# Performance work log

Measured on AMD Instinct MI355X. Metric: run time of the kernel, lower is better.

## Reference

```python
import jax, jax.numpy as jnp
import numpy as np

B, T, I, H, L = 256, 512, 64, 256, 2


def _lstm_layer(x, Wih, Whh, bih, bhh):
    # x: [B, T, Din]; Wih: [4H, Din]; Whh: [4H, H]; gate order i,f,g,o (PyTorch)
    Hdim = Whh.shape[1]
    # Precompute input projections for all timesteps (one big GEMM)
    x_proj = jnp.einsum('btd,gd->btg', x, Wih) + bih + bhh  # [B, T, 4H]
    x_proj = jnp.transpose(x_proj, (1, 0, 2))  # [T, B, 4H]

    def step(carry, xt):
        h, c = carry
        gates = xt + h @ Whh.T  # [B, 4H]
        i, f, g, o = jnp.split(gates, 4, axis=-1)
        i = jax.nn.sigmoid(i)
        f = jax.nn.sigmoid(f)
        g = jnp.tanh(g)
        o = jax.nn.sigmoid(o)
        c = f * c + i * g
        h = o * jnp.tanh(c)
        return (h, c), h

    b = x.shape[0]
    h0 = jnp.zeros((b, Hdim), dtype=x.dtype)
    c0 = jnp.zeros((b, Hdim), dtype=x.dtype)
    _, hs = jax.lax.scan(step, (h0, c0), x_proj)  # hs: [T, B, H]
    return jnp.transpose(hs, (1, 0, 2))  # [B, T, H]


def setup_inputs() -> dict:
    key = jax.random.key(0)
    ks = jax.random.split(key, 12)
    s_in = 1.0 / np.sqrt(H)
    inp = {
        'x': jax.random.normal(ks[0], (B, T, I), dtype=jnp.float32),
        'Wih0': jax.random.uniform(ks[1], (4 * H, I), minval=-s_in, maxval=s_in),
        'Whh0': jax.random.uniform(ks[2], (4 * H, H), minval=-s_in, maxval=s_in),
        'bih0': jax.random.uniform(ks[3], (4 * H,), minval=-s_in, maxval=s_in),
        'bhh0': jax.random.uniform(ks[4], (4 * H,), minval=-s_in, maxval=s_in),
        'Wih1': jax.random.uniform(ks[5], (4 * H, H), minval=-s_in, maxval=s_in),
        'Whh1': jax.random.uniform(ks[6], (4 * H, H), minval=-s_in, maxval=s_in),
        'bih1': jax.random.uniform(ks[7], (4 * H,), minval=-s_in, maxval=s_in),
        'bhh1': jax.random.uniform(ks[8], (4 * H,), minval=-s_in, maxval=s_in),
        'Wfc': jax.random.uniform(ks[9], (1, H), minval=-s_in, maxval=s_in),
        'bfc': jax.random.uniform(ks[10], (1,), minval=-s_in, maxval=s_in),
    }
    return inp


def reference(x, Wih0, Whh0, bih0, bhh0, Wih1, Whh1, bih1, bhh1, Wfc, bfc):
    h1 = _lstm_layer(x, Wih0, Whh0, bih0, bhh0)   # [B, T, H]
    h2 = _lstm_layer(h1, Wih1, Whh1, bih1, bhh1)  # [B, T, H]
    last = h2[:, -1, :]                           # [B, H]
    return last @ Wfc.T + bfc                     # [B, 1]
```

## Files before the change

### kernel.cpp

```cpp
#include <hip/hip_runtime.h>

#define TT   512
#define IDIM 64
#define HDIM 256

typedef short  short8  __attribute__((ext_vector_type(8)));
typedef short  short4v __attribute__((ext_vector_type(4)));
typedef float  f32x4   __attribute__((ext_vector_type(4)));
typedef unsigned int       u32;
typedef unsigned long long u64;

__device__ __forceinline__ short f2bf(float f) {
    unsigned u = __float_as_uint(f);
    u = u + 0x7FFFu + ((u >> 16) & 1u);
    return (short)(u >> 16);
}
__device__ __forceinline__ u32 f2bf_u(float f) {
    unsigned u = __float_as_uint(f);
    u = u + 0x7FFFu + ((u >> 16) & 1u);
    return (u >> 16);
}
__device__ __forceinline__ float bf2f(short h) {
    return __uint_as_float(((unsigned)(unsigned short)h) << 16);
}
__device__ __forceinline__ float sigm(float x)  { return 1.0f / (1.0f + __expf(-x)); }
__device__ __forceinline__ float tanh_(float x) { return 2.0f / (1.0f + __expf(-2.0f * x)) - 1.0f; }

__global__ __launch_bounds__(256, 1) void lstm_fused(
    const float* __restrict__ x,
    const float* __restrict__ Wih0, const float* __restrict__ Whh0,
    const float* __restrict__ bih0, const float* __restrict__ bhh0,
    const float* __restrict__ Wih1, const float* __restrict__ Whh1,
    const float* __restrict__ bih1, const float* __restrict__ bhh1,
    const float* __restrict__ Wfc,  const float* __restrict__ bfc,
    float* __restrict__ out, char* __restrict__ ws)
{
    u32* h0w = (u32*)ws;
    u32* h1w = h0w + 2 * 16 * 16 * 256;

    const int blk   = blockIdx.x;
    const int grp   = ((blk & 7) << 1) | ((blk >> 3) & 1);
    const int chunk = blk >> 4;
    const int tid   = threadIdx.x;
    const int lane  = tid & 63;
    const int wave  = tid >> 6;
    const int quad  = lane >> 4;
    const int nn    = lane & 15;

    __shared__ short A0[16][328];
    __shared__ short A1[16][520];
    __shared__ float gbuf[2][4][16][16];
    __shared__ float red[16][16];
    __shared__ float ldspad[13312];

    for (int i = tid; i < 16 * 328; i += 256) (&A0[0][0])[i] = 0;
    for (int i = tid; i < 16 * 520; i += 256) (&A1[0][0])[i] = 0;

    const int wrow = wave * HDIM + chunk * 16 + nn;
    short8 w0f[10];
    short8 w1f[16];
#pragma unroll
    for (int kb = 0; kb < 10; ++kb)
#pragma unroll
        for (int j = 0; j < 8; ++j) {
            int k = kb * 32 + quad * 8 + j;
            float v = (k < 64) ? Wih0[wrow * IDIM + k] : Whh0[wrow * HDIM + (k - 64)];
            w0f[kb][j] = f2bf(v);
        }
#pragma unroll
    for (int kb = 0; kb < 16; ++kb)
#pragma unroll
        for (int j = 0; j < 8; ++j) {
            int k = kb * 32 + quad * 8 + j;
            float v = (k < 256) ? Wih1[wrow * HDIM + k] : Whh1[wrow * HDIM + (k - 256)];
            w1f[kb][j] = f2bf(v);
        }
    const float bias0 = bih0[wrow] + bhh0[wrow];
    const float bias1 = bih1[wrow] + bhh1[wrow];

    const int em = tid >> 4;
    const int ej = tid & 15;
    float c0 = 0.0f, c1 = 0.0f;

    auto load_x = [&](int t) {
        const float4 v = *(const float4*)&x[((size_t)(grp * 16 + em) * TT + t) * IDIM + ej * 4];
        short4v sv;
        sv[0] = f2bf(v.x); sv[1] = f2bf(v.y); sv[2] = f2bf(v.z); sv[3] = f2bf(v.w);
        *(short4v*)&A0[em][ej * 4] = sv;
    };

    __syncthreads();
    load_x(0);
    __syncthreads();

    for (int s = 0; s <= TT; ++s) {
        const int par = s & 1;
        const u32 tag = (u32)(s + 1);

        if (s < TT) {
            f32x4 acc = {0.f, 0.f, 0.f, 0.f};
#pragma unroll
            for (int kb = 0; kb < 10; ++kb) {
                short8 a = *(const short8*)&A0[nn][kb * 32 + quad * 8];
                acc = __builtin_amdgcn_mfma_f32_16x16x32_bf16(a, w0f[kb], acc, 0, 0, 0);
            }
#pragma unroll
            for (int r = 0; r < 4; ++r)
                gbuf[0][wave][quad * 4 + r][nn] = acc[r] + bias0;
        }
        if (s >= 1) {
            f32x4 acc = {0.f, 0.f, 0.f, 0.f};
#pragma unroll
            for (int kb = 0; kb < 16; ++kb) {
                short8 a = *(const short8*)&A1[nn][kb * 32 + quad * 8];
                acc = __builtin_amdgcn_mfma_f32_16x16x32_bf16(a, w1f[kb], acc, 0, 0, 0);
            }
#pragma unroll
            for (int r = 0; r < 4; ++r)
                gbuf[1][wave][quad * 4 + r][nn] = acc[r] + bias1;
        }
        __syncthreads();

        const size_t wbase = ((size_t)(par * 16 + grp) * 16 + em) * 256 + chunk * 16 + ej;
        if (s < TT) {
            float gi = sigm (gbuf[0][0][em][ej]);
            float gf = sigm (gbuf[0][1][em][ej]);
            float gg = tanh_(gbuf[0][2][em][ej]);
            float go = sigm (gbuf[0][3][em][ej]);
            c0 = gf * c0 + gi * gg;
            u32 hb = f2bf_u(go * tanh_(c0));
            __hip_atomic_store(&h0w[wbase], (hb << 16) | tag,
                               __ATOMIC_RELAXED, __HIP_MEMORY_SCOPE_AGENT);
        }
        {
            u32 hb = 0;
            if (s >= 1) {
                float gi = sigm (gbuf[1][0][em][ej]);
                float gf = sigm (gbuf[1][1][em][ej]);
                float gg = tanh_(gbuf[1][2][em][ej]);
                float go = sigm (gbuf[1][3][em][ej]);
                c1 = gf * c1 + gi * gg;
                hb = f2bf_u(go * tanh_(c1));
            }
            __hip_atomic_store(&h1w[wbase], (hb << 16) | tag,
                               __ATOMIC_RELAXED, __HIP_MEMORY_SCOPE_AGENT);
        }

        if (s + 1 < TT) load_x(s + 1);

        const size_t rbase = ((size_t)(par * 16 + grp) * 16 + em) * 256 + ej * 16;
        u64* p0 = (u64*)&h0w[rbase];
        u64* p1 = (u64*)&h1w[rbase];
        u64 r0[8], r1[8];
        const bool need0 = (s < TT);
        for (;;) {
            u32 bad = 0;
            if (need0) {
#pragma unroll
                for (int i = 0; i < 8; ++i)
                    r0[i] = __hip_atomic_load(&p0[i], __ATOMIC_RELAXED, __HIP_MEMORY_SCOPE_AGENT);
            }
#pragma unroll
            for (int i = 0; i < 8; ++i)
                r1[i] = __hip_atomic_load(&p1[i], __ATOMIC_RELAXED, __HIP_MEMORY_SCOPE_AGENT);
            if (need0) {
#pragma unroll
                for (int i = 0; i < 8; ++i)
                    bad |= (((u32)r0[i] ^ tag) & 0xFFFFu) | ((((u32)(r0[i] >> 32)) ^ tag) & 0xFFFFu);
            }
#pragma unroll
            for (int i = 0; i < 8; ++i)
                bad |= (((u32)r1[i] ^ tag) & 0xFFFFu) | ((((u32)(r1[i] >> 32)) ^ tag) & 0xFFFFu);
            if (!bad) break;
        }

        if (need0) {
            u32 w[8];
#pragma unroll
            for (int i = 0; i < 8; ++i) {
                u32 lo = (u32)r0[i], hi = (u32)(r0[i] >> 32);
                w[i] = (lo >> 16) | (hi & 0xFFFF0000u);
            }
            uint4 q0 = {w[0], w[1], w[2], w[3]};
            uint4 q1 = {w[4], w[5], w[6], w[7]};
            *(uint4*)&A0[em][64 + ej * 16]     = q0;
            *(uint4*)&A0[em][64 + ej * 16 + 8] = q1;
            *(uint4*)&A1[em][ej * 16]          = q0;
            *(uint4*)&A1[em][ej * 16 + 8]      = q1;
        }
        {
            u32 w[8];
#pragma unroll
            for (int i = 0; i < 8; ++i) {
                u32 lo = (u32)r1[i], hi = (u32)(r1[i] >> 32);
                w[i] = (lo >> 16) | (hi & 0xFFFF0000u);
            }
            uint4 q0 = {w[0], w[1], w[2], w[3]};
            uint4 q1 = {w[4], w[5], w[6], w[7]};
            *(uint4*)&A1[em][256 + ej * 16]     = q0;
            *(uint4*)&A1[em][256 + ej * 16 + 8] = q1;
        }
        __syncthreads();
    }

    {
        float part = 0.f;
#pragma unroll
        for (int kk = 0; kk < 16; ++kk) {
            int k = ej * 16 + kk;
            part += bf2f(A1[em][256 + k]) * Wfc[k];
        }
        red[em][ej] = part;
    }
    __syncthreads();
    if (chunk == 0 && tid < 16) {
        float sum = bfc[0];
#pragma unroll
        for (int c = 0; c < 16; ++c) sum += red[tid][c];
        out[grp * 16 + tid] = sum;
    }

    if (gridDim.x > 100000) { ldspad[tid] = bias0; out[0] = ldspad[255 - tid]; }
}

extern "C" void kernel_launch(void* const* d_in, const int* in_sizes, int n_in,
                              void* d_out, int out_size, void* d_ws, size_t ws_size,
                              hipStream_t stream) {
    (void)in_sizes; (void)n_in; (void)out_size; (void)ws_size;
    const float* x    = (const float*)d_in[0];
    const float* Wih0 = (const float*)d_in[1];
    const float* Whh0 = (const float*)d_in[2];
    const float* bih0 = (const float*)d_in[3];
    const float* bhh0 = (const float*)d_in[4];
    const float* Wih1 = (const float*)d_in[5];
    const float* Whh1 = (const float*)d_in[6];
    const float* bih1 = (const float*)d_in[7];
    const float* bhh1 = (const float*)d_in[8];
    const float* Wfc  = (const float*)d_in[9];
    const float* bfc  = (const float*)d_in[10];

    lstm_fused<<<256, 256, 0, stream>>>(x, Wih0, Whh0, bih0, bhh0,
                                        Wih1, Whh1, bih1, bhh1, Wfc, bfc,
                                        (float*)d_out, (char*)d_ws);
}
```

Baseline: 1.875 ms.

## Interleave two batch groups per block to hide cross-block h exchange latency

```diff
diff --git a/kernel.cpp b/kernel.cpp
--- a/kernel.cpp
+++ b/kernel.cpp
@@ -39,22 +39,21 @@
     u32* h1w = h0w + 2 * 16 * 16 * 256;
 
     const int blk   = blockIdx.x;
-    const int grp   = ((blk & 7) << 1) | ((blk >> 3) & 1);
-    const int chunk = blk >> 4;
+    const int g8    = blk & 7;
+    const int chunk = blk >> 3;
     const int tid   = threadIdx.x;
     const int lane  = tid & 63;
     const int wave  = tid >> 6;
     const int quad  = lane >> 4;
     const int nn    = lane & 15;
 
-    __shared__ short A0[16][328];
-    __shared__ short A1[16][520];
-    __shared__ float gbuf[2][4][16][16];
+    __shared__ short A0[2][16][328];
+    __shared__ short A1[2][16][520];
+    __shared__ float gbuf[2][4][16][17];
     __shared__ float red[16][16];
-    __shared__ float ldspad[13312];
-
-    for (int i = tid; i < 16 * 328; i += 256) (&A0[0][0])[i] = 0;
-    for (int i = tid; i < 16 * 520; i += 256) (&A1[0][0])[i] = 0;
+
+    for (int i = tid; i < 2 * 16 * 328; i += 256) (&A0[0][0][0])[i] = 0;
+    for (int i = tid; i < 2 * 16 * 520; i += 256) (&A1[0][0][0])[i] = 0;
 
     const int wrow = wave * HDIM + chunk * 16 + nn;
     short8 w0f[10];
@@ -80,147 +79,168 @@
 
     const int em = tid >> 4;
     const int ej = tid & 15;
-    float c0 = 0.0f, c1 = 0.0f;
-
-    auto load_x = [&](int t) {
-        const float4 v = *(const float4*)&x[((size_t)(grp * 16 + em) * TT + t) * IDIM + ej * 4];
+    float c0[2] = {0.f, 0.f}, c1[2] = {0.f, 0.f};
+
+#pragma unroll
+    for (int ctx = 0; ctx < 2; ++ctx) {
+        const int grp = g8 + 8 * ctx;
+        const float4 v = *(const float4*)&x[((size_t)(grp * 16 + em) * TT + 0) * IDIM + ej * 4];
         short4v sv;
         sv[0] = f2bf(v.x); sv[1] = f2bf(v.y); sv[2] = f2bf(v.z); sv[3] = f2bf(v.w);
-        *(short4v*)&A0[em][ej * 4] = sv;
-    };
-
+        *(short4v*)&A0[ctx][em][ej * 4] = sv;
+    }
     __syncthreads();
-    load_x(0);
-    __syncthreads();
 
     for (int s = 0; s <= TT; ++s) {
-        const int par = s & 1;
-        const u32 tag = (u32)(s + 1);
-
-        if (s < TT) {
-            f32x4 acc = {0.f, 0.f, 0.f, 0.f};
-#pragma unroll
-            for (int kb = 0; kb < 10; ++kb) {
-                short8 a = *(const short8*)&A0[nn][kb * 32 + quad * 8];
-                acc = __builtin_amdgcn_mfma_f32_16x16x32_bf16(a, w0f[kb], acc, 0, 0, 0);
-            }
-#pragma unroll
-            for (int r = 0; r < 4; ++r)
-                gbuf[0][wave][quad * 4 + r][nn] = acc[r] + bias0;
-        }
-        if (s >= 1) {
-            f32x4 acc = {0.f, 0.f, 0.f, 0.f};
-#pragma unroll
-            for (int kb = 0; kb < 16; ++kb) {
-                short8 a = *(const short8*)&A1[nn][kb * 32 + quad * 8];
-                acc = __builtin_amdgcn_mfma_f32_16x16x32_bf16(a, w1f[kb], acc, 0, 0, 0);
-            }
-#pragma unroll
-            for (int r = 0; r < 4; ++r)
-                gbuf[1][wave][quad * 4 + r][nn] = acc[r] + bias1;
-        }
-        __syncthreads();
-
-        const size_t wbase = ((size_t)(par * 16 + grp) * 16 + em) * 256 + chunk * 16 + ej;
-        if (s < TT) {
-            float gi = sigm (gbuf[0][0][em][ej]);
-            float gf = sigm (gbuf[0][1][em][ej]);
-            float gg = tanh_(gbuf[0][2][em][ej]);
-            float go = sigm (gbuf[0][3][em][ej]);
-            c0 = gf * c0 + gi * gg;
-            u32 hb = f2bf_u(go * tanh_(c0));
-            __hip_atomic_store(&h0w[wbase], (hb << 16) | tag,
-                               __ATOMIC_RELAXED, __HIP_MEMORY_SCOPE_AGENT);
-        }
-        {
-            u32 hb = 0;
+        const u32 tag  = (u32)s;
+        const u32 ptag = (u32)(s + 1);
+        const int rpar = (s - 1) & 1;
+        const int wpar = s & 1;
+
+        for (int ctx = 0; ctx < 2; ++ctx) {
+            const int grp = g8 + 8 * ctx;
+
+            float4 xv;
+            const bool xpre = (s + 1 < TT);
+            if (xpre)
+                xv = *(const float4*)&x[((size_t)(grp * 16 + em) * TT + (s + 1)) * IDIM + ej * 4];
+
             if (s >= 1) {
-                float gi = sigm (gbuf[1][0][em][ej]);
-                float gf = sigm (gbuf[1][1][em][ej]);
-                float gg = tanh_(gbuf[1][2][em][ej]);
-                float go = sigm (gbuf[1][3][em][ej]);
-                c1 = gf * c1 + gi * gg;
-                hb = f2bf_u(go * tanh_(c1));
-            }
-            __hip_atomic_store(&h1w[wbase], (hb << 16) | tag,
-                               __ATOMIC_RELAXED, __HIP_MEMORY_SCOPE_AGENT);
-        }
-
-        if (s + 1 < TT) load_x(s + 1);
-
-        const size_t rbase = ((size_t)(par * 16 + grp) * 16 + em) * 256 + ej * 16;
-        u64* p0 = (u64*)&h0w[rbase];
+                const size_t rbase = ((size_t)(rpar * 16 + grp) * 16 + em) * 256 + ej * 16;
+                u64* p0 = (u64*)&h0w[rbase];
+                u64* p1 = (u64*)&h1w[rbase];
+                u64 r0[8], r1[8];
+                for (;;) {
+                    u32 bad = 0;
+#pragma unroll
+                    for (int i = 0; i < 8; ++i)
+                        r0[i] = __hip_atomic_load(&p0[i], __ATOMIC_RELAXED, __HIP_MEMORY_SCOPE_AGENT);
+#pragma unroll
+                    for (int i = 0; i < 8; ++i)
+                        r1[i] = __hip_atomic_load(&p1[i], __ATOMIC_RELAXED, __HIP_MEMORY_SCOPE_AGENT);
+#pragma unroll
+                    for (int i = 0; i < 8; ++i)
+                        bad |= (((u32)r0[i] ^ tag) & 0xFFFFu) | ((((u32)(r0[i] >> 32)) ^ tag) & 0xFFFFu)
+                             | (((u32)r1[i] ^ tag) & 0xFFFFu) | ((((u32)(r1[i] >> 32)) ^ tag) & 0xFFFFu);
+                    if (!bad) break;
+                }
+                u32 w[8];
+#pragma unroll
+                for (int i = 0; i < 8; ++i) {
+                    u32 lo = (u32)r0[i], hi = (u32)(r0[i] >> 32);
+                    w[i] = (lo >> 16) | (hi & 0xFFFF0000u);
+                }
+                {
+                    uint4 q0 = {w[0], w[1], w[2], w[3]};
+                    uint4 q1 = {w[4], w[5], w[6], w[7]};
+                    *(uint4*)&A0[ctx][em][64 + ej * 16]     = q0;
+                    *(uint4*)&A0[ctx][em][64 + ej * 16 + 8] = q1;
+                    *(uint4*)&A1[ctx][em][ej * 16]          = q0;
+                    *(uint4*)&A1[ctx][em][ej * 16 + 8]      = q1;
+                }
+#pragma unroll
+                for (int i = 0; i < 8; ++i) {
+                    u32 lo = (u32)r1[i], hi = (u32)(r1[i] >> 32);
+                    w[i] = (lo >> 16) | (hi & 0xFFFF0000u);
+                }
+                {
+                    uint4 q0 = {w[0], w[1], w[2], w[3]};
+                    uint4 q1 = {w[4], w[5], w[6], w[7]};
+                    *(uint4*)&A1[ctx][em][256 + ej * 16]     = q0;
+                    *(uint4*)&A1[ctx][em][256 + ej * 16 + 8] = q1;
+                }
+            }
+            __syncthreads();
+
+            if (s < TT) {
+                f32x4 acc = {0.f, 0.f, 0.f, 0.f};
+#pragma unroll
+                for (int kb = 0; kb < 10; ++kb) {
+                    short8 a = *(const short8*)&A0[ctx][nn][kb * 32 + quad * 8];
+                    acc = __builtin_amdgcn_mfma_f32_16x16x32_bf16(a, w0f[kb], acc, 0, 0, 0);
+                }
+#pragma unroll
+                for (int r = 0; r < 4; ++r)
+                    gbuf[0][wave][quad * 4 + r][nn] = acc[r] + bias0;
+            }
+            if (s >= 1) {
+                f32x4 acc = {0.f, 0.f, 0.f, 0.f};
+#pragma unroll
+                for (int kb = 0; kb < 16; ++kb) {
+                    short8 a = *(const short8*)&A1[ctx][nn][kb * 32 + quad * 8];
+                    acc = __builtin_amdgcn_mfma_f32_16x16x32_bf16(a, w1f[kb], acc, 0, 0, 0);
+                }
+#pragma unroll
+                for (int r = 0; r < 4; ++r)
+                    gbuf[1][wave][quad * 4 + r][nn] = acc[r] + bias1;
+            }
+            __syncthreads();
+
+            const size_t wbase = ((size_t)(wpar * 16 + grp) * 16 + em) * 256 + chunk * 16 + ej;
+            if (s < TT) {
+                float gi = sigm (gbuf[0][0][em][ej]);
+                float gf = sigm (gbuf[0][1][em][ej]);
+                float gg = tanh_(gbuf[0][2][em][ej]);
+                float go = sigm (gbuf[0][3][em][ej]);
+                c0[ctx] = gf * c0[ctx] + gi * gg;
+                u32 hb = f2bf_u(go * tanh_(c0[ctx]));
+                __hip_atomic_store(&h0w[wbase], (hb << 16) | ptag,
+                                   __ATOMIC_RELAXED, __HIP_MEMORY_SCOPE_AGENT);
+            }
+            {
+                u32 hb = 0;
+                if (s >= 1) {
+                    float gi = sigm (gbuf[1][0][em][ej]);
+                    float gf = sigm (gbuf[1][1][em][ej]);
+                    float gg = tanh_(gbuf[1][2][em][ej]);
+                    float go = sigm (gbuf[1][3][em][ej]);
+                    c1[ctx] = gf * c1[ctx] + gi * gg;
+                    hb = f2bf_u(go * tanh_(c1[ctx]));
+                }
+                __hip_atomic_store(&h1w[wbase], (hb << 16) | ptag,
+                                   __ATOMIC_RELAXED, __HIP_MEMORY_SCOPE_AGENT);
+            }
+            if (xpre) {
+                short4v sv;
+                sv[0] = f2bf(xv.x); sv[1] = f2bf(xv.y); sv[2] = f2bf(xv.z); sv[3] = f2bf(xv.w);
+                *(short4v*)&A0[ctx][em][ej * 4] = sv;
+            }
+        }
+    }
+
+    for (int ctx = 0; ctx < 2; ++ctx) {
+        const int grp = g8 + 8 * ctx;
+        const u32 ftag = (u32)(TT + 1);
+        const size_t rbase = ((size_t)((TT & 1) * 16 + grp) * 16 + em) * 256 + ej * 16;
         u64* p1 = (u64*)&h1w[rbase];
-        u64 r0[8], r1[8];
-        const bool need0 = (s < TT);
+        u64 r1[8];
         for (;;) {
             u32 bad = 0;
-            if (need0) {
-#pragma unroll
-                for (int i = 0; i < 8; ++i)
-                    r0[i] = __hip_atomic_load(&p0[i], __ATOMIC_RELAXED, __HIP_MEMORY_SCOPE_AGENT);
-            }
 #pragma unroll
             for (int i = 0; i < 8; ++i)
                 r1[i] = __hip_atomic_load(&p1[i], __ATOMIC_RELAXED, __HIP_MEMORY_SCOPE_AGENT);
-            if (need0) {
-#pragma unroll
-                for (int i = 0; i < 8; ++i)
-                    bad |= (((u32)r0[i] ^ tag) & 0xFFFFu) | ((((u32)(r0[i] >> 32)) ^ tag) & 0xFFFFu);
-            }
 #pragma unroll
             for (int i = 0; i < 8; ++i)
-                bad |= (((u32)r1[i] ^ tag) & 0xFFFFu) | ((((u32)(r1[i] >> 32)) ^ tag) & 0xFFFFu);
+                bad |= (((u32)r1[i] ^ ftag) & 0xFFFFu) | ((((u32)(r1[i] >> 32)) ^ ftag) & 0xFFFFu);
             if (!bad) break;
         }
-
-        if (need0) {
-            u32 w[8];
-#pragma unroll
-            for (int i = 0; i < 8; ++i) {
-                u32 lo = (u32)r0[i], hi = (u32)(r0[i] >> 32);
-                w[i] = (lo >> 16) | (hi & 0xFFFF0000u);
-            }
-            uint4 q0 = {w[0], w[1], w[2], w[3]};
-            uint4 q1 = {w[4], w[5], w[6], w[7]};
-            *(uint4*)&A0[em][64 + ej * 16]     = q0;
-            *(uint4*)&A0[em][64 + ej * 16 + 8] = q1;
-            *(uint4*)&A1[em][ej * 16]          = q0;
-            *(uint4*)&A1[em][ej * 16 + 8]      = q1;
-        }
-        {
-            u32 w[8];
-#pragma unroll
-            for (int i = 0; i < 8; ++i) {
-                u32 lo = (u32)r1[i], hi = (u32)(r1[i] >> 32);
-                w[i] = (lo >> 16) | (hi & 0xFFFF0000u);
-            }
-            uint4 q0 = {w[0], w[1], w[2], w[3]};
-            uint4 q1 = {w[4], w[5], w[6], w[7]};
-            *(uint4*)&A1[em][256 + ej * 16]     = q0;
-            *(uint4*)&A1[em][256 + ej * 16 + 8] = q1;
+        float part = 0.f;
+#pragma unroll
+        for (int i = 0; i < 8; ++i) {
+            u32 lo = (u32)r1[i], hi = (u32)(r1[i] >> 32);
+            part += bf2f((short)(lo >> 16)) * Wfc[ej * 16 + 2 * i];
+            part += bf2f((short)(hi >> 16)) * Wfc[ej * 16 + 2 * i + 1];
+        }
+        red[em][ej] = part;
+        __syncthreads();
+        if (chunk == 0 && tid < 16) {
+            float sum = bfc[0];
+#pragma unroll
+            for (int c = 0; c < 16; ++c) sum += red[tid][c];
+            out[grp * 16 + tid] = sum;
         }
         __syncthreads();
     }
-
-    {
-        float part = 0.f;
-#pragma unroll
-        for (int kk = 0; kk < 16; ++kk) {
-            int k = ej * 16 + kk;
-            part += bf2f(A1[em][256 + k]) * Wfc[k];
-        }
-        red[em][ej] = part;
-    }
-    __syncthreads();
-    if (chunk == 0 && tid < 16) {
-        float sum = bfc[0];
-#pragma unroll
-        for (int c = 0; c < 16; ++c) sum += red[tid][c];
-        out[grp * 16 + tid] = sum;
-    }
-
-    if (gridDim.x > 100000) { ldspad[tid] = bias0; out[0] = ldspad[255 - tid]; }
 }
 
 extern "C" void kernel_launch(void* const* d_in, const int* in_sizes, int n_in,
@@ -239,7 +259,7 @@
     const float* Wfc  = (const float*)d_in[9];
     const float* bfc  = (const float*)d_in[10];
 
-    lstm_fused<<<256, 256, 0, stream>>>(x, Wih0, Whh0, bih0, bhh0,
+    lstm_fused<<<128, 256, 0, stream>>>(x, Wih0, Whh0, bih0, bhh0,
                                         Wih1, Whh1, bih1, bhh1, Wfc, bfc,
                                         (float*)d_out, (char*)d_ws);
 }
```

New measurement: 3.120 ms. 66.4% more time.

## Use XCD-local workgroup-scope fast exchange path with agent-scope fallback for hidden state

Applied to the files above, without the earlier changes.

```diff
diff --git a/kernel.cpp b/kernel.cpp
--- a/kernel.cpp
+++ b/kernel.cpp
@@ -3,10 +3,12 @@
 #define TT   512
 #define IDIM 64
 #define HDIM 256
+#define FAST_TRIES 96
 
 typedef short  short8  __attribute__((ext_vector_type(8)));
 typedef short  short4v __attribute__((ext_vector_type(4)));
 typedef float  f32x4   __attribute__((ext_vector_type(4)));
+typedef int    int4v   __attribute__((ext_vector_type(4)));
 typedef unsigned int       u32;
 typedef unsigned long long u64;
 
@@ -35,12 +37,12 @@
     const float* __restrict__ Wfc,  const float* __restrict__ bfc,
     float* __restrict__ out, char* __restrict__ ws)
 {
-    u32* h0w = (u32*)ws;
-    u32* h1w = h0w + 2 * 16 * 16 * 256;
+    u64* hfast = (u64*)ws;
+    u64* hslow = (u64*)(ws + 1024 * 1024);
 
     const int blk   = blockIdx.x;
-    const int grp   = ((blk & 7) << 1) | ((blk >> 3) & 1);
-    const int chunk = blk >> 4;
+    const int grp   = (blk & 7) + 8 * (blk >> 7);
+    const int chunk = (blk >> 3) & 15;
     const int tid   = threadIdx.x;
     const int lane  = tid & 63;
     const int wave  = tid >> 6;
@@ -49,9 +51,9 @@
 
     __shared__ short A0[16][328];
     __shared__ short A1[16][520];
-    __shared__ float gbuf[2][4][16][16];
+    __shared__ float gbuf[2][4][16][17];
     __shared__ float red[16][16];
-    __shared__ float ldspad[13312];
+    __shared__ float ldspad[12288];
 
     for (int i = tid; i < 16 * 328; i += 256) (&A0[0][0])[i] = 0;
     for (int i = tid; i < 16 * 520; i += 256) (&A1[0][0])[i] = 0;
@@ -81,6 +83,7 @@
     const int em = tid >> 4;
     const int ej = tid & 15;
     float c0 = 0.0f, c1 = 0.0f;
+    bool useFast = true;
 
     auto load_x = [&](int t) {
         const float4 v = *(const float4*)&x[((size_t)(grp * 16 + em) * TT + t) * IDIM + ej * 4];
@@ -89,7 +92,6 @@
         *(short4v*)&A0[em][ej * 4] = sv;
     };
 
-    __syncthreads();
     load_x(0);
     __syncthreads();
 
@@ -121,84 +123,101 @@
         }
         __syncthreads();
 
-        const size_t wbase = ((size_t)(par * 16 + grp) * 16 + em) * 256 + chunk * 16 + ej;
+        u32 h0word = tag, h1word = tag;
         if (s < TT) {
             float gi = sigm (gbuf[0][0][em][ej]);
             float gf = sigm (gbuf[0][1][em][ej]);
             float gg = tanh_(gbuf[0][2][em][ej]);
             float go = sigm (gbuf[0][3][em][ej]);
             c0 = gf * c0 + gi * gg;
-            u32 hb = f2bf_u(go * tanh_(c0));
-            __hip_atomic_store(&h0w[wbase], (hb << 16) | tag,
-                               __ATOMIC_RELAXED, __HIP_MEMORY_SCOPE_AGENT);
-        }
+            h0word = (f2bf_u(go * tanh_(c0)) << 16) | tag;
+        }
+        if (s >= 1) {
+            float gi = sigm (gbuf[1][0][em][ej]);
+            float gf = sigm (gbuf[1][1][em][ej]);
+            float gg = tanh_(gbuf[1][2][em][ej]);
+            float go = sigm (gbuf[1][3][em][ej]);
+            c1 = gf * c1 + gi * gg;
+            h1word = (f2bf_u(go * tanh_(c1)) << 16) | tag;
+        }
+        const u64 pub  = ((u64)h1word << 32) | (u64)h0word;
+        const size_t widx = ((size_t)(par * 16 + grp) * 16 + em) * 256 + chunk * 16 + ej;
+        __hip_atomic_store(&hfast[widx], pub, __ATOMIC_RELAXED, __HIP_MEMORY_SCOPE_WORKGROUP);
+        __hip_atomic_store(&hslow[widx], pub, __ATOMIC_RELAXED, __HIP_MEMORY_SCOPE_AGENT);
+
+        if (s + 1 < TT) load_x(s + 1);
+
+        const size_t ridx = ((size_t)(par * 16 + grp) * 16 + em) * 256 + ej * 16;
+        int4v q[8];
+        bool got = false;
+        if (useFast) {
+            const u64* rp = &hfast[ridx];
+            for (int trial = 0; trial < FAST_TRIES && !got; ++trial) {
+                asm volatile(
+                    "global_load_dwordx4 %0, %8, off sc0\n\t"
+                    "global_load_dwordx4 %1, %8, off offset:16 sc0\n\t"
+                    "global_load_dwordx4 %2, %8, off offset:32 sc0\n\t"
+                    "global_load_dwordx4 %3, %8, off offset:48 sc0\n\t"
+                    "global_load_dwordx4 %4, %8, off offset:64 sc0\n\t"
+                    "global_load_dwordx4 %5, %8, off offset:80 sc0\n\t"
+                    "global_load_dwordx4 %6, %8, off offset:96 sc0\n\t"
+                    "global_load_dwordx4 %7, %8, off offset:112 sc0\n\t"
+                    "s_waitcnt vmcnt(0)"
+                    : "=&v"(q[0]), "=&v"(q[1]), "=&v"(q[2]), "=&v"(q[3]),
+                      "=&v"(q[4]), "=&v"(q[5]), "=&v"(q[6]), "=&v"(q[7])
+                    : "v"(rp)
+                    : "memory");
+                u32 bad = 0;
+#pragma unroll
+                for (int i = 0; i < 8; ++i)
+                    bad |= (((u32)q[i][0] ^ tag) & 0xFFFFu) | (((u32)q[i][1] ^ tag) & 0xFFFFu)
+                         | (((u32)q[i][2] ^ tag) & 0xFFFFu) | (((u32)q[i][3] ^ tag) & 0xFFFFu);
+                got = (bad == 0);
+            }
+            if (!got) useFast = false;
+        }
+        if (!got) {
+            const u64* rp = &hslow[ridx];
+            for (;;) {
+                u64 r[16];
+#pragma unroll
+                for (int i = 0; i < 16; ++i)
+                    r[i] = __hip_atomic_load(&rp[i], __ATOMIC_RELAXED, __HIP_MEMORY_SCOPE_AGENT);
+                u32 bad = 0;
+#pragma unroll
+                for (int i = 0; i < 16; ++i)
+                    bad |= (((u32)r[i] ^ tag) & 0xFFFFu)
+                         | ((((u32)(r[i] >> 32)) ^ tag) & 0xFFFFu);
+                if (!bad) {
+#pragma unroll
+                    for (int i = 0; i < 8; ++i) {
+                        q[i][0] = (int)(u32)r[2 * i];
+                        q[i][1] = (int)(u32)(r[2 * i] >> 32);
+                        q[i][2] = (int)(u32)r[2 * i + 1];
+                        q[i][3] = (int)(u32)(r[2 * i + 1] >> 32);
+                    }
+                    break;
+                }
+            }
+        }
+
         {
-            u32 hb = 0;
-            if (s >= 1) {
-                float gi = sigm (gbuf[1][0][em][ej]);
-                float gf = sigm (gbuf[1][1][em][ej]);
-                float gg = tanh_(gbuf[1][2][em][ej]);
-                float go = sigm (gbuf[1][3][em][ej]);
-                c1 = gf * c1 + gi * gg;
-                hb = f2bf_u(go * tanh_(c1));
-            }
-            __hip_atomic_store(&h1w[wbase], (hb << 16) | tag,
-                               __ATOMIC_RELAXED, __HIP_MEMORY_SCOPE_AGENT);
-        }
-
-        if (s + 1 < TT) load_x(s + 1);
-
-        const size_t rbase = ((size_t)(par * 16 + grp) * 16 + em) * 256 + ej * 16;
-        u64* p0 = (u64*)&h0w[rbase];
-        u64* p1 = (u64*)&h1w[rbase];
-        u64 r0[8], r1[8];
-        const bool need0 = (s < TT);
-        for (;;) {
-            u32 bad = 0;
-            if (need0) {
-#pragma unroll
-                for (int i = 0; i < 8; ++i)
-                    r0[i] = __hip_atomic_load(&p0[i], __ATOMIC_RELAXED, __HIP_MEMORY_SCOPE_AGENT);
-            }
-#pragma unroll
-            for (int i = 0; i < 8; ++i)
-                r1[i] = __hip_atomic_load(&p1[i], __ATOMIC_RELAXED, __HIP_MEMORY_SCOPE_AGENT);
-            if (need0) {
-#pragma unroll
-                for (int i = 0; i < 8; ++i)
-                    bad |= (((u32)r0[i] ^ tag) & 0xFFFFu) | ((((u32)(r0[i] >> 32)) ^ tag) & 0xFFFFu);
-            }
-#pragma unroll
-            for (int i = 0; i < 8; ++i)
-                bad |= (((u32)r1[i] ^ tag) & 0xFFFFu) | ((((u32)(r1[i] >> 32)) ^ tag) & 0xFFFFu);
-            if (!bad) break;
-        }
-
-        if (need0) {
-            u32 w[8];
+            u32 w0[8], w1[8];
 #pragma unroll
             for (int i = 0; i < 8; ++i) {
-                u32 lo = (u32)r0[i], hi = (u32)(r0[i] >> 32);
-                w[i] = (lo >> 16) | (hi & 0xFFFF0000u);
-            }
-            uint4 q0 = {w[0], w[1], w[2], w[3]};
-            uint4 q1 = {w[4], w[5], w[6], w[7]};
+                w0[i] = (((u32)q[i][0]) >> 16) | (((u32)q[i][2]) & 0xFFFF0000u);
+                w1[i] = (((u32)q[i][1]) >> 16) | (((u32)q[i][3]) & 0xFFFF0000u);
+            }
+            uint4 q0 = {w0[0], w0[1], w0[2], w0[3]};
+            uint4 q1 = {w0[4], w0[5], w0[6], w0[7]};
             *(uint4*)&A0[em][64 + ej * 16]     = q0;
             *(uint4*)&A0[em][64 + ej * 16 + 8] = q1;
             *(uint4*)&A1[em][ej * 16]          = q0;
             *(uint4*)&A1[em][ej * 16 + 8]      = q1;
-        }
-        {
-            u32 w[8];
-#pragma unroll
-            for (int i = 0; i < 8; ++i) {
-                u32 lo = (u32)r1[i], hi = (u32)(r1[i] >> 32);
-                w[i] = (lo >> 16) | (hi & 0xFFFF0000u);
-            }
-            uint4 q0 = {w[0], w[1], w[2], w[3]};
-            uint4 q1 = {w[4], w[5], w[6], w[7]};
-            *(uint4*)&A1[em][256 + ej * 16]     = q0;
-            *(uint4*)&A1[em][256 + ej * 16 + 8] = q1;
+            uint4 q2 = {w1[0], w1[1], w1[2], w1[3]};
+            uint4 q3 = {w1[4], w1[5], w1[6], w1[7]};
+            *(uint4*)&A1[em][256 + ej * 16]     = q2;
+            *(uint4*)&A1[em][256 + ej * 16 + 8] = q3;
         }
         __syncthreads();
     }
```

Measured after the change: 3.580 ms. 1.91x slower.
